# Kernel tuning notes

Measured on AMD Instinct MI355X. Metric: run time of the kernel, lower is better.

## Reference

```python
import jax, jax.numpy as jnp
import numpy as np

N = 100000
MAX_HOPS = 3
EPS = 1e-16


def _gat_conv(x, src, dst, W, a_src, a_dst, bias, heads, out_c, concat):
    """PyG-style GATConv (eval mode, self-loops, negative_slope=0.2)."""
    n = x.shape[0]
    loop = jnp.arange(n, dtype=src.dtype)
    s = jnp.concatenate([src, loop])
    d = jnp.concatenate([dst, loop])
    h = (x @ W).reshape(n, heads, out_c)                      # [N,H,C]
    al_s = (h * a_src).sum(-1)                                # [N,H]
    al_d = (h * a_dst).sum(-1)                                # [N,H]
    e = jax.nn.leaky_relu(al_s[s] + al_d[d], 0.2)             # [E,H]
    e_max = jax.ops.segment_max(e, d, num_segments=n)
    e = jnp.exp(e - e_max[d])
    denom = jax.ops.segment_sum(e, d, num_segments=n)
    alpha = e / (denom[d] + EPS)                              # edge softmax per dst
    out = jax.ops.segment_sum(h[s] * alpha[:, :, None], d, num_segments=n)  # [N,H,C]
    out = out.reshape(n, heads * out_c) if concat else out.mean(axis=1)
    return out + bias


def _hierarchy(src, dst, seed, n, max_hops):
    """BFS hop distance from seeds; one-hot rows, all-zero if unreached."""
    reached = seed
    dist = jnp.where(seed, 0, max_hops + 1)
    for h in range(1, max_hops + 1):
        msg = jax.ops.segment_max(reached[src].astype(jnp.int32), dst, num_segments=n)
        nbr = msg > 0
        dist = jnp.where(nbr & (~reached), h, dist)
        reached = reached | nbr
    mask = (dist[:, None] == jnp.arange(max_hops + 1)[None, :]).astype(jnp.float32)
    hop_counts = jnp.argmax(mask, axis=1).astype(jnp.float32)  # all-zero row -> 0, like torch
    return mask, hop_counts


def setup_inputs() -> dict:
    key = jax.random.key(0)
    ks = jax.random.split(key, 20)
    in_aug = 128 + MAX_HOPS + 1  # 132
    out_channels = 40
    g = lambda k, shp: (jax.random.normal(k, shp, dtype=jnp.float32) * 0.1)
    return {
        "x": jax.random.normal(ks[0], (N, 128), dtype=jnp.float32),
        "edge_index": jax.random.randint(ks[1], (2, 1600000), 0, N, dtype=jnp.int64),
        "seed_mask": jax.random.randint(ks[2], (N,), 0, 100, dtype=jnp.int32),
        "W1": g(ks[3], (in_aug, 8 * 8)), "a1s": g(ks[4], (8, 8)), "a1d": g(ks[5], (8, 8)), "b1": jnp.zeros((64,), jnp.float32),
        "W2": g(ks[6], (64, 8 * 16)), "a2s": g(ks[7], (8, 16)), "a2d": g(ks[8], (8, 16)), "b2": jnp.zeros((128,), jnp.float32),
        "W3": g(ks[9], (128, out_channels)), "a3s": g(ks[10], (1, out_channels)), "a3d": g(ks[11], (1, out_channels)), "b3": jnp.zeros((out_channels,), jnp.float32),
        "Wg": g(ks[12], (129, 1)), "bg": jnp.zeros((1,), jnp.float32),
    }


def reference(x, edge_index, seed_mask, W1, a1s, a1d, b1, W2, a2s, a2d, b2,
              W3, a3s, a3d, b3, Wg, bg):
    src, dst = edge_index[0], edge_index[1]
    seed = seed_mask == 0
    hmask, hop_counts = _hierarchy(src, dst, seed, N, MAX_HOPS)
    aug = jnp.concatenate([x, hmask], axis=1)
    h1 = jax.nn.elu(_gat_conv(aug, src, dst, W1, a1s, a1d, b1, 8, 8, True))
    h2 = _gat_conv(h1, src, dst, W2, a2s, a2d, b2, 8, 16, True)
    gate_in = jnp.concatenate([h2, hop_counts[:, None]], axis=1)
    gate = jax.nn.sigmoid(gate_in @ Wg + bg)
    h2 = h2 * gate
    h3 = _gat_conv(h2, src, dst, W3, a3s, a3d, b3, 1, 40, False)
    return jax.nn.log_softmax(h3, axis=1)
```

## Files before the change

kernel.cpp:

```cpp
#include <hip/hip_runtime.h>
#include <hip/hip_bf16.h>
#include <hip/hip_fp16.h>
#include <math.h>

#define MAXH 3
#define NSB 9
#define NS (1 << NSB)
#define SRCBITS 17
#define SRCMASK ((1 << SRCBITS) - 1)
#define LOG2E 1.4426950408889634f
typedef unsigned int u32;
typedef unsigned char u8;
typedef unsigned short u16;

using bf16x8 = __attribute__((ext_vector_type(8))) short;
using f32x4  = __attribute__((ext_vector_type(4))) float;

__device__ __forceinline__ float lrelu2(float x) { return fmaxf(x, 0.2f * x); }
__device__ __forceinline__ float fexp2(float x) {
#if __has_builtin(__builtin_amdgcn_exp2f)
    return __builtin_amdgcn_exp2f(x);
#else
    return exp2f(x);
#endif
}
__device__ __forceinline__ u16 f2bf(float f) {
    u32 u = __float_as_uint(f);
    u32 r = ((u >> 16) & 1u) + 0x7fffu;
    return (u16)((u + r) >> 16);
}

__global__ void k_bfs_init(const int* __restrict__ seed_mask, int* dist, int n) {
    int i = blockIdx.x * blockDim.x + threadIdx.x;
    if (i < n) dist[i] = (seed_mask[i] == 0) ? 0 : (MAXH + 1);
}
__global__ void k_rbits_init(const int* __restrict__ seed_mask, u32* rbits, int nw, int n) {
    int w = blockIdx.x * blockDim.x + threadIdx.x;
    if (w < nw) {
        u32 b = 0;
        int base = w * 32;
        int lim = min(32, n - base);
        for (int j = 0; j < lim; j++)
            if (seed_mask[base + j] == 0) b |= (1u << j);
        rbits[w] = b;
    }
}
__global__ void k_bfs_scan(const int* __restrict__ rowptr, const int* __restrict__ csr_src,
                           const u32* __restrict__ rbits, u8* __restrict__ nbr, int n) {
    int i = blockIdx.x * blockDim.x + threadIdx.x;
    if (i < n) {
        if (!((rbits[i >> 5] >> (i & 31)) & 1u)) {
            int beg = rowptr[i], end = rowptr[i + 1];
            u8 f = 0;
            for (int k = beg; k < end; k++) {
                int s = csr_src[k];
                if ((rbits[s >> 5] >> (s & 31)) & 1u) { f = 1; break; }
            }
            nbr[i] = f;
        }
    }
}
__global__ void k_bfs_node(u32* rbits, int* dist, const u8* __restrict__ nbr, int h, int n) {
    int i = blockIdx.x * blockDim.x + threadIdx.x;
    if (i < n) {
        if (nbr[i] && !((rbits[i >> 5] >> (i & 31)) & 1u)) {
            dist[i] = h;
            atomicOr(&rbits[i >> 5], 1u << (i & 31));
        }
    }
}

__global__ void k_bincount(const int4* __restrict__ dst4, int* bincnt, int E4) {
    __shared__ int cnt[256];
    int t = threadIdx.x;
    cnt[t] = 0;
    __syncthreads();
    int i = blockIdx.x * 256 + t;
    if (i < E4) {
        int4 d = dst4[i];
        atomicAdd(&cnt[d.x >> NSB], 1);
        atomicAdd(&cnt[d.y >> NSB], 1);
        atomicAdd(&cnt[d.z >> NSB], 1);
        atomicAdd(&cnt[d.w >> NSB], 1);
    }
    __syncthreads();
    if (cnt[t] > 0) atomicAdd(&bincnt[t], cnt[t]);
}

__global__ void k_binscan(const int* __restrict__ bincnt, int* binbase, int* bincur,
                          int* rowptr, int BINS, int E, int n) {
    __shared__ int sd[256];
    int t = threadIdx.x;
    int v = (t < BINS) ? bincnt[t] : 0;
    sd[t] = v;
    __syncthreads();
    for (int off = 1; off < 256; off <<= 1) {
        int add = (t >= off) ? sd[t - off] : 0;
        __syncthreads();
        sd[t] += add;
        __syncthreads();
    }
    int excl = sd[t] - v;
    if (t < BINS) { binbase[t] = excl; bincur[t] = excl; }
    if (t == 0) { binbase[BINS] = E; rowptr[n] = E; }
}

__global__ void k_binscatter(const int4* __restrict__ src4, const int4* __restrict__ dst4,
                             int* bincur, int* __restrict__ pairs, int E4, int BINS) {
    __shared__ int cnt[256], base[256];
    int t = threadIdx.x;
    cnt[t] = 0;
    __syncthreads();
    int i = blockIdx.x * 256 + t;
    int bin[4], rank[4], pack[4];
    bool valid = i < E4;
    if (valid) {
        int4 s = src4[i], d = dst4[i];
        bin[0] = d.x >> NSB; pack[0] = ((d.x & (NS - 1)) << SRCBITS) | s.x;
        bin[1] = d.y >> NSB; pack[1] = ((d.y & (NS - 1)) << SRCBITS) | s.y;
        bin[2] = d.z >> NSB; pack[2] = ((d.z & (NS - 1)) << SRCBITS) | s.z;
        bin[3] = d.w >> NSB; pack[3] = ((d.w & (NS - 1)) << SRCBITS) | s.w;
        rank[0] = atomicAdd(&cnt[bin[0]], 1);
        rank[1] = atomicAdd(&cnt[bin[1]], 1);
        rank[2] = atomicAdd(&cnt[bin[2]], 1);
        rank[3] = atomicAdd(&cnt[bin[3]], 1);
    }
    __syncthreads();
    if (t < BINS && cnt[t] > 0) base[t] = atomicAdd(&bincur[t], cnt[t]);
    __syncthreads();
    if (valid) {
        pairs[base[bin[0]] + rank[0]] = pack[0];
        pairs[base[bin[1]] + rank[1]] = pack[1];
        pairs[base[bin[2]] + rank[2]] = pack[2];
        pairs[base[bin[3]] + rank[3]] = pack[3];
    }
}

__global__ void k_binsort(const int* __restrict__ pairs, const int* __restrict__ binbase,
                          int* __restrict__ rowptr, int* __restrict__ csr_src, int n) {
    __shared__ int hist[NS];
    const int b = blockIdx.x, t = threadIdx.x;
    const int nbeg = b << NSB;
    const int ebeg = binbase[b];
    const int ecnt = binbase[b + 1] - ebeg;
    hist[t] = 0; hist[t + 256] = 0;
    __syncthreads();
    for (int i = t; i < ecnt; i += 256)
        atomicAdd(&hist[(u32)pairs[ebeg + i] >> SRCBITS], 1);
    for (int d = 1; d < NS; d <<= 1) {
        __syncthreads();
        int idx = (t + 1) * (d << 1) - 1;
        if (idx < NS) hist[idx] += hist[idx - d];
    }
    __syncthreads();
    if (t == 0) hist[NS - 1] = 0;
    for (int d = NS / 2; d >= 1; d >>= 1) {
        __syncthreads();
        int idx = (t + 1) * (d << 1) - 1;
        if (idx < NS) { int tmp = hist[idx - d]; hist[idx - d] = hist[idx]; hist[idx] += tmp; }
    }
    __syncthreads();
    int g0 = nbeg + t, g1 = nbeg + t + 256;
    if (g0 < n) rowptr[g0] = ebeg + hist[t];
    if (g1 < n) rowptr[g1] = ebeg + hist[t + 256];
    __syncthreads();
    for (int i = t; i < ecnt; i += 256) {
        int p = pairs[ebeg + i];
        int pos = atomicAdd(&hist[(u32)p >> SRCBITS], 1);
        csr_src[ebeg + pos] = p & SRCMASK;
    }
}

template <int K, int KW, int MP, int MREAL, int AH, int AC, int THREADS>
__launch_bounds__(THREADS)
__global__ void k_gemm_t(const float* __restrict__ A, const float* __restrict__ W,
                         const float* __restrict__ a_s, const float* __restrict__ a_d,
                         const int* __restrict__ dist, __half* __restrict__ out,
                         float* __restrict__ als, float* __restrict__ ald, int n) {
    constexpr int COLT = MP / 4;
    constexpr int ROWT = THREADS / COLT;
    constexpr int RPT = 64 / ROWT;
    constexpr int BK = 64;
    constexpr int SAP = BK + 4;
    __shared__ float sA[64 * SAP];
    __shared__ float sW[KW * MP];

    for (int i = threadIdx.x; i < KW * MP; i += THREADS) {
        int r = i / MP, c = i % MP;
        sW[i] = (c < MREAL) ? W[r * MREAL + c] : 0.0f;
    }
    const int tcol = threadIdx.x % COLT;
    const int trow = threadIdx.x / COLT;
    const int rowbase = blockIdx.x * 64;

    float4 acc[RPT];
#pragma unroll
    for (int r = 0; r < RPT; r++) acc[r] = float4{0.f, 0.f, 0.f, 0.f};

    for (int k0 = 0; k0 < K; k0 += BK) {
        __syncthreads();
        for (int i = threadIdx.x; i < 64 * (BK / 4); i += THREADS) {
            int r = i / (BK / 4), c4 = i % (BK / 4);
            int row = rowbase + r;
            float4 v = float4{0.f, 0.f, 0.f, 0.f};
            if (row < n) v = *(const float4*)&A[(size_t)row * K + k0 + c4 * 4];
            *(float4*)&sA[r * SAP + c4 * 4] = v;
        }
        __syncthreads();
#pragma unroll 2
        for (int k4 = 0; k4 < BK / 4; k4++) {
            float4 w0 = *(const float4*)&sW[(k0 + k4 * 4 + 0) * MP + tcol * 4];
            float4 w1 = *(const float4*)&sW[(k0 + k4 * 4 + 1) * MP + tcol * 4];
            float4 w2 = *(const float4*)&sW[(k0 + k4 * 4 + 2) * MP + tcol * 4];
            float4 w3 = *(const float4*)&sW[(k0 + k4 * 4 + 3) * MP + tcol * 4];
#pragma unroll
            for (int r = 0; r < RPT; r++) {
                float4 a = *(const float4*)&sA[(trow * RPT + r) * SAP + k4 * 4];
                acc[r].x += a.x * w0.x + a.y * w1.x + a.z * w2.x + a.w * w3.x;
                acc[r].y += a.x * w0.y + a.y * w1.y + a.z * w2.y + a.w * w3.y;
                acc[r].z += a.x * w0.z + a.y * w1.z + a.z * w2.z + a.w * w3.z;
                acc[r].w += a.x * w0.w + a.y * w1.w + a.z * w2.w + a.w * w3.w;
            }
        }
    }

    float as_[4], ad_[4];
#pragma unroll
    for (int j = 0; j < 4; j++) {
        int col = tcol * 4 + j;
        bool ok = col < MREAL;
        as_[j] = ok ? a_s[col] * LOG2E : 0.0f;
        ad_[j] = ok ? a_d[col] * LOG2E : 0.0f;
    }
    constexpr int TPH = AC / 4;
    constexpr int RW = (TPH & (TPH - 1)) ? 16 : TPH;
    const int head = (tcol * 4) / AC;

#pragma unroll
    for (int r = 0; r < RPT; r++) {
        int row = rowbase + trow * RPT + r;
        if (row < n) {
            int d = dist[row];
            if (d <= MAXH) {
                float4 wd = *(const float4*)&sW[(K + d) * MP + tcol * 4];
                acc[r].x += wd.x; acc[r].y += wd.y; acc[r].z += wd.z; acc[r].w += wd.w;
            }
        }
        float ps = acc[r].x * as_[0] + acc[r].y * as_[1] + acc[r].z * as_[2] + acc[r].w * as_[3];
        float pd = acc[r].x * ad_[0] + acc[r].y * ad_[1] + acc[r].z * ad_[2] + acc[r].w * ad_[3];
#pragma unroll
        for (int o = 1; o < RW; o <<= 1) {
            ps += __shfl_xor(ps, o);
            pd += __shfl_xor(pd, o);
        }
        if (row < n) {
            if ((tcol % RW) == 0) {
                als[(size_t)row * AH + head] = ps;
                ald[(size_t)row * AH + head] = pd;
            }
            if (tcol * 4 + 3 < MREAL) {
                __half2* op = (__half2*)&out[(size_t)row * MREAL + tcol * 4];
                op[0] = __floats2half2_rn(acc[r].x, acc[r].y);
                op[1] = __floats2half2_rn(acc[r].z, acc[r].w);
            }
        }
    }
}

template <int K, int NREAL, int NTT, int AH, int C, int SK, int MBW>
__launch_bounds__(256)
__global__ void k_gemm_mfma(const u16* __restrict__ A, const float* __restrict__ W,
                            const float* __restrict__ a_s, const float* __restrict__ a_d,
                            __half* __restrict__ out, float* __restrict__ als,
                            float* __restrict__ ald, int n) {
    constexpr int KT = K / 32;
    constexpr int NTCOL = (NTT - 1) * 16;
    __shared__ u16 WT[NTT * 16 * SK];
    for (int idx = threadIdx.x; idx < NTT * 16 * K; idx += 256) {
        int c = idx / K, k = idx % K;
        float v = 0.0f;
        if (c < NREAL) {
            v = W[k * NREAL + c];
        } else if (c >= NTCOL && c < NTCOL + 2 * AH) {
            int j = (c - NTCOL) % AH;
            const float* aw = (c < NTCOL + AH) ? a_s : a_d;
            float accv = 0.0f;
            for (int cc = 0; cc < C; cc++) accv += W[k * NREAL + j * C + cc] * aw[j * C + cc];
            v = accv * LOG2E;
        }
        WT[c * SK + k] = f2bf(v);
    }
    __syncthreads();

    const int lane = threadIdx.x & 63;
    const int l15 = lane & 15;
    const int kg = lane >> 4;
    const int wid = blockIdx.x * 4 + (threadIdx.x >> 6);

    bf16x8 bfr[NTT][KT];
#pragma unroll
    for (int nt = 0; nt < NTT; nt++)
#pragma unroll
        for (int kt = 0; kt < KT; kt++)
            bfr[nt][kt] = *(const bf16x8*)&WT[(nt * 16 + l15) * SK + kt * 32 + kg * 8];

    for (int mb = 0; mb < MBW; mb++) {
        const int rowbase = (wid * MBW + mb) * 16;
        if (rowbase >= n) break;
        bf16x8 af[KT];
#pragma unroll
        for (int kt = 0; kt < KT; kt++)
            af[kt] = *(const bf16x8*)&A[(size_t)(rowbase + l15) * K + kt * 32 + kg * 8];
        f32x4 acc[NTT];
#pragma unroll
        for (int nt = 0; nt < NTT; nt++) acc[nt] = f32x4{0.f, 0.f, 0.f, 0.f};
#pragma unroll
        for (int kt = 0; kt < KT; kt++)
#pragma unroll
            for (int nt = 0; nt < NTT; nt++)
                acc[nt] = __builtin_amdgcn_mfma_f32_16x16x32_bf16(af[kt], bfr[nt][kt],
                                                                  acc[nt], 0, 0, 0);
#pragma unroll
        for (int nt = 0; nt < NTT - 1; nt++) {
            int c = nt * 16 + l15;
            if (c < NREAL) {
#pragma unroll
                for (int r = 0; r < 4; r++) {
                    int row = rowbase + kg * 4 + r;
                    out[(size_t)row * NREAL + c] = __float2half(acc[nt][r]);
                }
            }
        }
#pragma unroll
        for (int r = 0; r < 4; r++) {
            int row = rowbase + kg * 4 + r;
            float v = acc[NTT - 1][r];
            if (l15 < AH) als[(size_t)row * AH + l15] = v;
            else if (l15 < 2 * AH) ald[(size_t)row * AH + (l15 - AH)] = v;
        }
    }
}

template <int H, int C, int CH, int MODE, typename OT>
__launch_bounds__(256)
__global__ void k_gat(const int* __restrict__ rowptr, const int* __restrict__ csr_src,
                      const __half* __restrict__ h, const float* __restrict__ als,
                      const float* __restrict__ ald, const float* __restrict__ bias,
                      const int* __restrict__ dist, const float* __restrict__ Wg,
                      const float* __restrict__ bg, OT* __restrict__ out, int n) {
    constexpr int TOT = H * C;
    constexpr int NL = TOT / CH;
    const int lane = threadIdx.x & 63;
    const int node = blockIdx.x * 4 + (threadIdx.x >> 6);
    if (node >= n) return;
    const int beg = rowptr[node];
    const int deg = rowptr[node + 1] - beg;

    const int cl = (lane < NL) ? lane : 0;
    const int hd = (cl * CH) / C;
    const float ald_hd = ald[(size_t)node * H + hd];
    const float m0 = lrelu2(als[(size_t)node * H + hd] + ald_hd);

    float s = 1.0f, ax, ay = 0.0f;
    if (CH == 2) {
        float2 hv = __half22float2(*(const __half2*)(h + (size_t)node * TOT + cl * 2));
        ax = hv.x; ay = hv.y;
    } else {
        ax = __half2float(h[(size_t)node * TOT + cl]);
    }

    auto body = [&](int sN) {
        float t = als[(size_t)sN * H + hd] + ald_hd;
        float p = fexp2(lrelu2(t) - m0);
        s += p;
        if (CH == 2) {
            float2 hf = __half22float2(*(const __half2*)(h + (size_t)sN * TOT + cl * 2));
            ax += p * hf.x;
            ay += p * hf.y;
        } else {
            ax += p * __half2float(h[(size_t)sN * TOT + cl]);
        }
    };

    for (int base = 0; base < deg; base += 64) {
        const int myE = base + lane;
        int sReg = (myE < deg) ? csr_src[beg + myE] : 0;
        const int cnt = min(64, deg - base);
        int e = 0;
        for (; e + 4 <= cnt; e += 4) {
            body(__builtin_amdgcn_readlane(sReg, e));
            body(__builtin_amdgcn_readlane(sReg, e + 1));
            body(__builtin_amdgcn_readlane(sReg, e + 2));
            body(__builtin_amdgcn_readlane(sReg, e + 3));
        }
        for (; e < cnt; e++) body(__builtin_amdgcn_readlane(sReg, e));
    }

    const float inv = 1.0f / (s + 1e-16f);
    float vx = ax * inv + bias[cl * CH];
    float vy = (CH == 2) ? (ay * inv + bias[cl * CH + 1]) : 0.0f;

    if (MODE == 1) {
        vx = vx > 0.0f ? vx : expm1f(vx);
        ((u16*)out)[(size_t)node * TOT + cl] = f2bf(vx);
    } else if (MODE == 2) {
        float2 wg = *(const float2*)&Wg[cl * 2];
        float part = vx * wg.x + vy * wg.y;
#pragma unroll
        for (int off = 32; off > 0; off >>= 1) part += __shfl_xor(part, off);
        int d = dist[node];
        float hop = (d <= MAXH) ? (float)d : 0.0f;
        float g = 1.0f / (1.0f + __expf(-(part + hop * Wg[128] + bg[0])));
        ushort2 w;
        w.x = f2bf(vx * g);
        w.y = f2bf(vy * g);
        *(ushort2*)&((u16*)out)[(size_t)node * TOT + cl * 2] = w;
    } else if (MODE == 3) {
        float v = (lane < NL) ? vx : -INFINITY;
        float mm = v;
#pragma unroll
        for (int off = 32; off > 0; off >>= 1) mm = fmaxf(mm, __shfl_xor(mm, off));
        float ex = (lane < NL) ? __expf(v - mm) : 0.0f;
        float ss = ex;
#pragma unroll
        for (int off = 32; off > 0; off >>= 1) ss += __shfl_xor(ss, off);
        float ls = logf(ss);
        if (lane < NL) ((float*)out)[(size_t)node * TOT + cl] = v - mm - ls;
    }
}

static inline int nblk(long long t, int b) { return (int)((t + b - 1) / b); }

extern "C" void kernel_launch(void* const* d_in, const int* in_sizes, int n_in,
                              void* d_out, int out_size, void* d_ws, size_t ws_size,
                              hipStream_t stream) {
    const float* x = (const float*)d_in[0];
    const int* eidx = (const int*)d_in[1];
    const int* seed_mask = (const int*)d_in[2];
    const float* W1 = (const float*)d_in[3];
    const float* a1s = (const float*)d_in[4];
    const float* a1d = (const float*)d_in[5];
    const float* b1 = (const float*)d_in[6];
    const float* W2 = (const float*)d_in[7];
    const float* a2s = (const float*)d_in[8];
    const float* a2d = (const float*)d_in[9];
    const float* b2 = (const float*)d_in[10];
    const float* W3 = (const float*)d_in[11];
    const float* a3s = (const float*)d_in[12];
    const float* a3d = (const float*)d_in[13];
    const float* b3 = (const float*)d_in[14];
    const float* Wg = (const float*)d_in[15];
    const float* bg = (const float*)d_in[16];

    const int n = in_sizes[0] / 128;
    const long long E = in_sizes[1] / 2;
    const int E4 = (int)(E / 4);
    const int4* src4 = (const int4*)eidx;
    const int4* dst4 = (const int4*)(eidx + E);
    const int BINS = (n + NS - 1) >> NSB;
    const int NW = (n + 31) / 32;

    char* ws = (char*)d_ws;
    size_t off = 0;
    auto alloc = [&](size_t bytes) -> void* {
        void* p = ws + off;
        off = (off + bytes + 255) & ~(size_t)255;
        return p;
    };
    int* dist    = (int*)alloc((size_t)n * 4);
    u32* rbits   = (u32*)alloc((size_t)NW * 4);
    u8* nbr      = (u8*)alloc((size_t)n);
    int* rowptr  = (int*)alloc((size_t)(n + 1) * 4);
    int* bincnt  = (int*)alloc(256 * 4);
    int* binbase = (int*)alloc(257 * 4);
    int* bincur  = (int*)alloc(256 * 4);
    int* csr_src = (int*)alloc((size_t)E * 4);
    float* als   = (float*)alloc((size_t)n * 8 * 4);
    float* ald   = (float*)alloc((size_t)n * 8 * 4);
    __half* hbuf = (__half*)alloc((size_t)n * 128 * 2);
    u16* abuf    = (u16*)alloc((size_t)n * 128 * 2);
    int* pairs   = (int*)abuf;
    float* out = (float*)d_out;

    const int BS = 256;

    hipMemsetAsync(bincnt, 0, 256 * 4, stream);
    k_bfs_init<<<nblk(n, BS), BS, 0, stream>>>(seed_mask, dist, n);
    k_rbits_init<<<nblk(NW, BS), BS, 0, stream>>>(seed_mask, rbits, NW, n);
    k_bincount<<<nblk(E4, BS), BS, 0, stream>>>(dst4, bincnt, E4);
    k_binscan<<<1, 256, 0, stream>>>(bincnt, binbase, bincur, rowptr, BINS, (int)E, n);
    k_binscatter<<<nblk(E4, BS), BS, 0, stream>>>(src4, dst4, bincur, pairs, E4, BINS);
    k_binsort<<<BINS, 256, 0, stream>>>(pairs, binbase, rowptr, csr_src, n);

    for (int h = 1; h <= MAXH; h++) {
        k_bfs_scan<<<nblk(n, BS), BS, 0, stream>>>(rowptr, csr_src, rbits, nbr, n);
        k_bfs_node<<<nblk(n, BS), BS, 0, stream>>>(rbits, dist, nbr, h, n);
    }

    const int mblocks = (n + 15) / 16;
    const int gmf = (mblocks + 15) / 16;

    k_gemm_t<128, 132, 64, 64, 8, 8, 256>
        <<<nblk(n, 64), 256, 0, stream>>>(x, W1, a1s, a1d, dist, hbuf, als, ald, n);
    k_gat<8, 8, 1, 1, u16><<<nblk(n, 4), 256, 0, stream>>>(
        rowptr, csr_src, hbuf, als, ald, b1, nullptr, nullptr, nullptr, abuf, n);

    k_gemm_mfma<64, 128, 9, 8, 16, 72, 4>
        <<<gmf, 256, 0, stream>>>(abuf, W2, a2s, a2d, hbuf, als, ald, n);
    k_gat<8, 16, 2, 2, u16><<<nblk(n, 4), 256, 0, stream>>>(
        rowptr, csr_src, hbuf, als, ald, b2, dist, Wg, bg, abuf, n);

    k_gemm_mfma<128, 40, 4, 1, 40, 136, 4>
        <<<gmf, 256, 0, stream>>>(abuf, W3, a3s, a3d, hbuf, als, ald, n);
    k_gat<1, 40, 1, 3, float><<<nblk(n, 4), 256, 0, stream>>>(
        rowptr, csr_src, hbuf, als, ald, b3, nullptr, nullptr, nullptr, out, n);
}
```

Baseline: 439.0 us.

## Use bf16 MFMA for first GAT projection and simplify edge-softmax inner loop

Replaces the fp32 SIMT GEMM for layer 1 with a bf16 MFMA kernel. The attention vectors are folded into extra weight columns, so the attention logits come out of the matrix multiply directly, and the hop one-hot columns are added as a per-row lookup. In the GAT aggregation loop, leaky-relu minus max is rewritten as a max of two affine terms with precomputed constants, and layer 2 accumulates in packed half2 FMA. This cuts ALU work in both kernels. The cost is lower precision: bf16 inputs for layer 1 and fp16 accumulation of weighted sums in layer 2, which may raise error or overflow.

```diff
diff --git a/kernel.cpp b/kernel.cpp
--- a/kernel.cpp
+++ b/kernel.cpp
@@ -16,7 +16,6 @@
 using bf16x8 = __attribute__((ext_vector_type(8))) short;
 using f32x4  = __attribute__((ext_vector_type(4))) float;
 
-__device__ __forceinline__ float lrelu2(float x) { return fmaxf(x, 0.2f * x); }
 __device__ __forceinline__ float fexp2(float x) {
 #if __has_builtin(__builtin_amdgcn_exp2f)
     return __builtin_amdgcn_exp2f(x);
@@ -171,98 +170,113 @@
     }
 }
 
-template <int K, int KW, int MP, int MREAL, int AH, int AC, int THREADS>
-__launch_bounds__(THREADS)
-__global__ void k_gemm_t(const float* __restrict__ A, const float* __restrict__ W,
-                         const float* __restrict__ a_s, const float* __restrict__ a_d,
-                         const int* __restrict__ dist, __half* __restrict__ out,
-                         float* __restrict__ als, float* __restrict__ ald, int n) {
-    constexpr int COLT = MP / 4;
-    constexpr int ROWT = THREADS / COLT;
-    constexpr int RPT = 64 / ROWT;
-    constexpr int BK = 64;
-    constexpr int SAP = BK + 4;
-    __shared__ float sA[64 * SAP];
-    __shared__ float sW[KW * MP];
-
-    for (int i = threadIdx.x; i < KW * MP; i += THREADS) {
-        int r = i / MP, c = i % MP;
-        sW[i] = (c < MREAL) ? W[r * MREAL + c] : 0.0f;
-    }
-    const int tcol = threadIdx.x % COLT;
-    const int trow = threadIdx.x / COLT;
-    const int rowbase = blockIdx.x * 64;
-
-    float4 acc[RPT];
-#pragma unroll
-    for (int r = 0; r < RPT; r++) acc[r] = float4{0.f, 0.f, 0.f, 0.f};
-
-    for (int k0 = 0; k0 < K; k0 += BK) {
-        __syncthreads();
-        for (int i = threadIdx.x; i < 64 * (BK / 4); i += THREADS) {
-            int r = i / (BK / 4), c4 = i % (BK / 4);
-            int row = rowbase + r;
-            float4 v = float4{0.f, 0.f, 0.f, 0.f};
-            if (row < n) v = *(const float4*)&A[(size_t)row * K + k0 + c4 * 4];
-            *(float4*)&sA[r * SAP + c4 * 4] = v;
-        }
-        __syncthreads();
-#pragma unroll 2
-        for (int k4 = 0; k4 < BK / 4; k4++) {
-            float4 w0 = *(const float4*)&sW[(k0 + k4 * 4 + 0) * MP + tcol * 4];
-            float4 w1 = *(const float4*)&sW[(k0 + k4 * 4 + 1) * MP + tcol * 4];
-            float4 w2 = *(const float4*)&sW[(k0 + k4 * 4 + 2) * MP + tcol * 4];
-            float4 w3 = *(const float4*)&sW[(k0 + k4 * 4 + 3) * MP + tcol * 4];
-#pragma unroll
-            for (int r = 0; r < RPT; r++) {
-                float4 a = *(const float4*)&sA[(trow * RPT + r) * SAP + k4 * 4];
-                acc[r].x += a.x * w0.x + a.y * w1.x + a.z * w2.x + a.w * w3.x;
-                acc[r].y += a.x * w0.y + a.y * w1.y + a.z * w2.y + a.w * w3.y;
-                acc[r].z += a.x * w0.z + a.y * w1.z + a.z * w2.z + a.w * w3.z;
-                acc[r].w += a.x * w0.w + a.y * w1.w + a.z * w2.w + a.w * w3.w;
+template <int SK, int MBW>
+__launch_bounds__(256)
+__global__ void k_gemm_mfma1(const float* __restrict__ A, const float* __restrict__ W,
+                             const float* __restrict__ a_s, const float* __restrict__ a_d,
+                             const int* __restrict__ dist, __half* __restrict__ out,
+                             float* __restrict__ als, float* __restrict__ ald, int n) {
+    constexpr int K = 128, NREAL = 64, NTT = 5, AH = 8, C = 8;
+    constexpr int KT = K / 32;
+    constexpr int NTCOL = (NTT - 1) * 16;
+    __shared__ u16 WT[NTT * 16 * SK];
+    __shared__ u16 sAW[4][16 * SK];
+    __shared__ float sAug[4][64];
+    __shared__ float sAugA[4][16];
+
+    for (int idx = threadIdx.x; idx < NTT * 16 * K; idx += 256) {
+        int c = idx / K, k = idx % K;
+        float v;
+        if (c < NREAL) {
+            v = W[k * NREAL + c];
+        } else {
+            int j = (c - NTCOL) & 7;
+            const float* aw = (c < NTCOL + AH) ? a_s : a_d;
+            float accv = 0.0f;
+            for (int cc = 0; cc < C; cc++) accv += W[k * NREAL + j * C + cc] * aw[j * C + cc];
+            v = accv * LOG2E;
+        }
+        WT[c * SK + k] = f2bf(v);
+    }
+    {
+        int t = threadIdx.x;
+        int d = t >> 6, c = t & 63;
+        sAug[d][c] = W[(K + d) * NREAL + c];
+        if (t < 64) {
+            int dd = t >> 4, j = t & 15;
+            int hh = j & 7;
+            const float* aw = (j < 8) ? a_s : a_d;
+            float accv = 0.0f;
+            for (int cc = 0; cc < C; cc++)
+                accv += W[(K + dd) * NREAL + hh * C + cc] * aw[hh * C + cc];
+            sAugA[dd][j] = accv * LOG2E;
+        }
+    }
+    __syncthreads();
+
+    const int lane = threadIdx.x & 63;
+    const int l15 = lane & 15;
+    const int kg = lane >> 4;
+    const int w = threadIdx.x >> 6;
+    const int wid = blockIdx.x * 4 + w;
+
+    bf16x8 bfr[NTT][KT];
+#pragma unroll
+    for (int nt = 0; nt < NTT; nt++)
+#pragma unroll
+        for (int kt = 0; kt < KT; kt++)
+            bfr[nt][kt] = *(const bf16x8*)&WT[(nt * 16 + l15) * SK + kt * 32 + kg * 8];
+
+    for (int mb = 0; mb < MBW; mb++) {
+        const int rowbase = (wid * MBW + mb) * 16;
+        if (rowbase >= n) break;
+        {
+            int r = lane >> 2, c4b = lane & 3;
+            const float* xr = A + (size_t)(rowbase + r) * K;
+#pragma unroll
+            for (int j = 0; j < 8; j++) {
+                int c4 = c4b + j * 4;
+                float4 v = *(const float4*)&xr[c4 * 4];
+                ushort4 o;
+                o.x = f2bf(v.x); o.y = f2bf(v.y); o.z = f2bf(v.z); o.w = f2bf(v.w);
+                *(ushort4*)&sAW[w][r * SK + c4 * 4] = o;
             }
         }
-    }
-
-    float as_[4], ad_[4];
-#pragma unroll
-    for (int j = 0; j < 4; j++) {
-        int col = tcol * 4 + j;
-        bool ok = col < MREAL;
-        as_[j] = ok ? a_s[col] * LOG2E : 0.0f;
-        ad_[j] = ok ? a_d[col] * LOG2E : 0.0f;
-    }
-    constexpr int TPH = AC / 4;
-    constexpr int RW = (TPH & (TPH - 1)) ? 16 : TPH;
-    const int head = (tcol * 4) / AC;
-
-#pragma unroll
-    for (int r = 0; r < RPT; r++) {
-        int row = rowbase + trow * RPT + r;
-        if (row < n) {
-            int d = dist[row];
-            if (d <= MAXH) {
-                float4 wd = *(const float4*)&sW[(K + d) * MP + tcol * 4];
-                acc[r].x += wd.x; acc[r].y += wd.y; acc[r].z += wd.z; acc[r].w += wd.w;
+        bf16x8 af[KT];
+#pragma unroll
+        for (int kt = 0; kt < KT; kt++)
+            af[kt] = *(const bf16x8*)&sAW[w][l15 * SK + kt * 32 + kg * 8];
+        f32x4 acc[NTT];
+#pragma unroll
+        for (int nt = 0; nt < NTT; nt++) acc[nt] = f32x4{0.f, 0.f, 0.f, 0.f};
+#pragma unroll
+        for (int kt = 0; kt < KT; kt++)
+#pragma unroll
+            for (int nt = 0; nt < NTT; nt++)
+                acc[nt] = __builtin_amdgcn_mfma_f32_16x16x32_bf16(af[kt], bfr[nt][kt],
+                                                                  acc[nt], 0, 0, 0);
+        int rows[4], dd[4];
+#pragma unroll
+        for (int r = 0; r < 4; r++) {
+            rows[r] = rowbase + kg * 4 + r;
+            dd[r] = dist[rows[r]];
+        }
+#pragma unroll
+        for (int nt = 0; nt < NTT - 1; nt++) {
+            int c = nt * 16 + l15;
+#pragma unroll
+            for (int r = 0; r < 4; r++) {
+                float v = acc[nt][r];
+                if (dd[r] <= MAXH) v += sAug[dd[r]][c];
+                out[(size_t)rows[r] * NREAL + c] = __float2half(v);
             }
         }
-        float ps = acc[r].x * as_[0] + acc[r].y * as_[1] + acc[r].z * as_[2] + acc[r].w * as_[3];
-        float pd = acc[r].x * ad_[0] + acc[r].y * ad_[1] + acc[r].z * ad_[2] + acc[r].w * ad_[3];
-#pragma unroll
-        for (int o = 1; o < RW; o <<= 1) {
-            ps += __shfl_xor(ps, o);
-            pd += __shfl_xor(pd, o);
-        }
-        if (row < n) {
-            if ((tcol % RW) == 0) {
-                als[(size_t)row * AH + head] = ps;
-                ald[(size_t)row * AH + head] = pd;
-            }
-            if (tcol * 4 + 3 < MREAL) {
-                __half2* op = (__half2*)&out[(size_t)row * MREAL + tcol * 4];
-                op[0] = __floats2half2_rn(acc[r].x, acc[r].y);
-                op[1] = __floats2half2_rn(acc[r].z, acc[r].w);
-            }
+#pragma unroll
+        for (int r = 0; r < 4; r++) {
+            float v = acc[NTT - 1][r];
+            if (dd[r] <= MAXH) v += sAugA[dd[r]][l15];
+            if (l15 < AH) als[(size_t)rows[r] * AH + l15] = v;
+            else ald[(size_t)rows[r] * AH + (l15 - AH)] = v;
         }
     }
 }
@@ -359,24 +373,28 @@
     const int cl = (lane < NL) ? lane : 0;
     const int hd = (cl * CH) / C;
     const float ald_hd = ald[(size_t)node * H + hd];
-    const float m0 = lrelu2(als[(size_t)node * H + hd] + ald_hd);
-
-    float s = 1.0f, ax, ay = 0.0f;
-    if (CH == 2) {
-        float2 hv = __half22float2(*(const __half2*)(h + (size_t)node * TOT + cl * 2));
-        ax = hv.x; ay = hv.y;
+    const float t0 = als[(size_t)node * H + hd] + ald_hd;
+    const float m0 = fmaxf(t0, 0.2f * t0);
+    const float c0 = ald_hd - m0;
+    const float c1 = 0.2f * ald_hd - m0;
+
+    float s = 1.0f;
+    float ax = 0.0f, ay = 0.0f;
+    __half2 acc2;
+    if (MODE == 2) {
+        acc2 = *(const __half2*)(h + (size_t)node * TOT + cl * 2);
     } else {
         ax = __half2float(h[(size_t)node * TOT + cl]);
     }
 
     auto body = [&](int sN) {
-        float t = als[(size_t)sN * H + hd] + ald_hd;
-        float p = fexp2(lrelu2(t) - m0);
+        float a = als[(size_t)sN * H + hd];
+        float v = fmaxf(a + c0, fmaf(a, 0.2f, c1));
+        float p = fexp2(v);
         s += p;
-        if (CH == 2) {
-            float2 hf = __half22float2(*(const __half2*)(h + (size_t)sN * TOT + cl * 2));
-            ax += p * hf.x;
-            ay += p * hf.y;
+        if (MODE == 2) {
+            __half2 ph = __float2half2_rn(p);
+            acc2 = __hfma2(ph, *(const __half2*)(h + (size_t)sN * TOT + cl * 2), acc2);
         } else {
             ax += p * __half2float(h[(size_t)sN * TOT + cl]);
         }
@@ -397,6 +415,10 @@
     }
 
     const float inv = 1.0f / (s + 1e-16f);
+    if (MODE == 2) {
+        float2 av = __half22float2(acc2);
+        ax = av.x; ay = av.y;
+    }
     float vx = ax * inv + bias[cl * CH];
     float vy = (CH == 2) ? (ay * inv + bias[cl * CH + 1]) : 0.0f;
 
@@ -411,10 +433,10 @@
         int d = dist[node];
         float hop = (d <= MAXH) ? (float)d : 0.0f;
         float g = 1.0f / (1.0f + __expf(-(part + hop * Wg[128] + bg[0])));
-        ushort2 w;
-        w.x = f2bf(vx * g);
-        w.y = f2bf(vy * g);
-        *(ushort2*)&((u16*)out)[(size_t)node * TOT + cl * 2] = w;
+        ushort2 wv;
+        wv.x = f2bf(vx * g);
+        wv.y = f2bf(vy * g);
+        *(ushort2*)&((u16*)out)[(size_t)node * TOT + cl * 2] = wv;
     } else if (MODE == 3) {
         float v = (lane < NL) ? vx : -INFINITY;
         float mm = v;
@@ -500,8 +522,8 @@
     const int mblocks = (n + 15) / 16;
     const int gmf = (mblocks + 15) / 16;
 
-    k_gemm_t<128, 132, 64, 64, 8, 8, 256>
-        <<<nblk(n, 64), 256, 0, stream>>>(x, W1, a1s, a1d, dist, hbuf, als, ald, n);
+    k_gemm_mfma1<136, 4>
+        <<<gmf, 256, 0, stream>>>(x, W1, a1s, a1d, dist, hbuf, als, ald, n);
     k_gat<8, 8, 1, 1, u16><<<nblk(n, 4), 256, 0, stream>>>(
         rowptr, csr_src, hbuf, als, ald, b1, nullptr, nullptr, nullptr, abuf, n);
 
```

After: 438.2 us. About the same (-0.2%).
